# Performance work log

Measured on AMD Instinct MI355X. Metric: run time of the kernel, lower is better.

The kernel has to match this reference:

```python
import jax, jax.numpy as jnp
import numpy as np

B, DIM, H, W = 1, 64, 128, 128
WS = 7  # window_size


def setup_inputs() -> dict:
    key = jax.random.key(0)
    ks = jax.random.split(key, 7)
    scale = 1.0 / np.sqrt(DIM).astype(np.float32)
    x = jax.random.normal(ks[0], (B, DIM, H, W), jnp.float32)
    Wq = jax.random.normal(ks[1], (DIM, DIM), jnp.float32) * scale
    bq = jax.random.normal(ks[2], (DIM,), jnp.float32) * 0.01
    Wk = jax.random.normal(ks[3], (DIM, DIM), jnp.float32) * scale
    bk = jax.random.normal(ks[4], (DIM,), jnp.float32) * 0.01
    Wv = jax.random.normal(ks[5], (DIM, DIM), jnp.float32) * scale
    bv = jax.random.normal(ks[6], (DIM,), jnp.float32) * 0.01
    return {"x": x, "Wq": Wq, "bq": bq, "Wk": Wk, "bk": bk, "Wv": Wv, "bv": bv}


def _conv1x1(x, Wt, b):
    # nn.Conv2d(dim, dim, kernel_size=1): out[b,o,h,w] = sum_c W[o,c]*x[b,c,h,w] + b[o]
    return jnp.einsum('bchw,oc->bohw', x, Wt) + b[None, :, None, None]


def _windows(t, ws):
    # zero-pad then extract ws x ws sliding windows -> (B, C, H, W, ws*ws)
    b, c, h, w = t.shape
    pad = ws // 2
    tp = jnp.pad(t, ((0, 0), (0, 0), (pad, pad), (pad, pad)))
    return jnp.stack([tp[:, :, i:i + h, j:j + w]
                      for i in range(ws) for j in range(ws)], axis=-1)


def reference(x, Wq, bq, Wk, bk, Wv, bv):
    q = _conv1x1(x, Wq, bq)
    k = _conv1x1(x, Wk, bk)
    v = _conv1x1(x, Wv, bv)
    qw = _windows(q, WS)  # (B,C,H,W,P)
    kw = _windows(k, WS)
    vw = _windows(v, WS)
    # row-wise attention: position (h,w) attends to (h,k) over width,
    # contracting channels and window taps p (exact math of the torch einsum)
    attn = jnp.einsum('bchwp,bchkp->bhwk', qw, kw)
    attn = jax.nn.softmax(attn, axis=-1)
    # fuse the weighted sum and the final sum over p into one einsum
    out = jnp.einsum('bhwk,bchkp->bchw', attn, vw)
    return out
```

## Files before the change

### kernel.cpp

```cpp
#include <hip/hip_runtime.h>

static constexpr int C    = 64;
static constexpr int H    = 128;
static constexpr int W    = 128;
static constexpr int NPIX = H * W;
static constexpr int PAD  = 3;

__global__ __launch_bounds__(256, 4) void k_conv(
    const float* __restrict__ x,
    const float* __restrict__ Wq, const float* __restrict__ bq,
    const float* __restrict__ Wk, const float* __restrict__ bk,
    const float* __restrict__ Wv, const float* __restrict__ bv,
    float* __restrict__ qT, float* __restrict__ ko, float* __restrict__ vo)
{
    const int tid  = threadIdx.x;
    const int lane = tid & 63;
    const int p    = blockIdx.x * 64 + lane;
    const int o0   = __builtin_amdgcn_readfirstlane(
                         blockIdx.y * 32 + (tid >> 6) * 8);
    const int z    = blockIdx.z;
    const float* Wm = (z == 0) ? Wq : (z == 1) ? Wk : Wv;
    const float* bm = (z == 0) ? bq : (z == 1) ? bk : bv;

    float xr[C];
#pragma unroll
    for (int c = 0; c < C; ++c) xr[c] = x[c * NPIX + p];

    float acc[8];
#pragma unroll
    for (int j = 0; j < 8; ++j) acc[j] = bm[o0 + j];

#pragma unroll
    for (int c = 0; c < C; ++c) {
        const float xv = xr[c];
#pragma unroll
        for (int j = 0; j < 8; ++j)
            acc[j] += Wm[(o0 + j) * C + c] * xv;
    }

    if (z == 0) {
        *(float4*)(qT + (size_t)p * C + o0) =
            make_float4(acc[0], acc[1], acc[2], acc[3]);
        *(float4*)(qT + (size_t)p * C + o0 + 4) =
            make_float4(acc[4], acc[5], acc[6], acc[7]);
    } else {
        float* outm = (z == 1) ? ko : vo;
#pragma unroll
        for (int j = 0; j < 8; ++j)
            outm[(o0 + j) * NPIX + p] = acc[j];
    }
}

__global__ __launch_bounds__(256, 4) void k_mid(
    const float* __restrict__ qT, const float* __restrict__ kmat,
    const float* __restrict__ v,
    float* __restrict__ Sd, float* __restrict__ Vs)
{
    __shared__ union {
        struct { float Sl[22][130]; float qs[22][64]; } g;
        struct { float vt[22][128]; float vh[22][128]; } box;
    } u;
    const int bid = blockIdx.x;
    const int tid = threadIdx.x;

    if (bid < 1024) {
        const int h   = bid >> 3;
        const int w0  = (bid & 7) * 16;
        const int kk  = tid & 127;
        const int wsl = tid >> 7;

        for (int i = tid; i < 22 * 16; i += 256) {
            int r  = i >> 4, c4 = (i & 15) << 2;
            int wp = w0 - 3 + r;
            float4 qv = make_float4(0.f, 0.f, 0.f, 0.f);
            if (wp >= 0 && wp < W)
                qv = *(const float4*)(qT + (size_t)(h * W + wp) * C + c4);
            *(float4*)(&u.g.qs[r][c4]) = qv;
        }

        float ksr[C];
#pragma unroll
        for (int c = 0; c < C; ++c) ksr[c] = kmat[c * NPIX + h * W + kk];
        __syncthreads();

        for (int j = 0; j < 11; ++j) {
            int row = wsl * 11 + j;
            float a0 = 0.f, a1 = 0.f, a2 = 0.f, a3 = 0.f;
#pragma unroll
            for (int c = 0; c < C; c += 4) {
                float4 qv = *(const float4*)(&u.g.qs[row][c]);
                a0 += qv.x * ksr[c + 0];
                a1 += qv.y * ksr[c + 1];
                a2 += qv.z * ksr[c + 2];
                a3 += qv.w * ksr[c + 3];
            }
            u.g.Sl[row][kk] = (a0 + a1) + (a2 + a3);
        }
        __syncthreads();

#pragma unroll
        for (int r = 0; r < 8; ++r) {
            int wl = wsl * 8 + r;
            float a = 0.f;
#pragma unroll
            for (int dd = -PAD; dd <= PAD; ++dd) {
                int kj = kk + dd;
                if (kj >= 0 && kj < W)
                    a += u.g.Sl[wl + 3 + dd][kj];
            }
            Sd[(size_t)(h * W + w0 + wl) * W + kk] = a;
        }
    } else {
        const int b2 = bid - 1024;
        const int c  = b2 >> 3;
        const int h0 = (b2 & 7) * 16;

        for (int i = tid; i < 22 * 128; i += 256) {
            int r = i >> 7, w = i & 127;
            int h = h0 - 3 + r;
            u.box.vt[r][w] = (h >= 0 && h < H) ? v[c * NPIX + h * W + w] : 0.f;
        }
        __syncthreads();
        for (int i = tid; i < 22 * 128; i += 256) {
            int r = i >> 7, w = i & 127;
            float s = 0.f;
#pragma unroll
            for (int d = -PAD; d <= PAD; ++d) {
                int wj = w + d;
                if (wj >= 0 && wj < W) s += u.box.vt[r][wj];
            }
            u.box.vh[r][w] = s;
        }
        __syncthreads();
        for (int i = tid; i < 16 * 128; i += 256) {
            int r = i >> 7, w = i & 127;
            float s = 0.f;
#pragma unroll
            for (int d = 0; d < 7; ++d) s += u.box.vh[r + d][w];
            Vs[c * NPIX + (h0 + r) * W + w] = s;
        }
    }
}

__global__ __launch_bounds__(256) void k_softmax(
    const float* __restrict__ Sd, float* __restrict__ attn)
{
    __shared__ float Sl[22][132];
    const int w   = blockIdx.x;
    const int h0  = blockIdx.y * 16;
    const int tid = threadIdx.x;

    for (int i = tid; i < 22 * 128; i += 256) {
        int r = i >> 7, kk = i & 127;
        int h = h0 - 3 + r;
        Sl[r][kk] = (h >= 0 && h < H)
                  ? Sd[(size_t)h * NPIX + w * W + kk] : 0.f;
    }
    __syncthreads();

    const int hl  = tid >> 4;
    const int sub = tid & 15;

    float lg[8];
#pragma unroll
    for (int r = 0; r < 8; ++r) {
        int kk = sub + 16 * r;
        float a = 0.f;
#pragma unroll
        for (int d = 0; d < 7; ++d) a += Sl[hl + d][kk];
        lg[r] = a;
    }

    float m = lg[0];
#pragma unroll
    for (int r = 1; r < 8; ++r) m = fmaxf(m, lg[r]);
#pragma unroll
    for (int off = 1; off <= 8; off <<= 1) m = fmaxf(m, __shfl_xor(m, off));
    float ssum = 0.f;
#pragma unroll
    for (int r = 0; r < 8; ++r) { lg[r] = __expf(lg[r] - m); ssum += lg[r]; }
#pragma unroll
    for (int off = 1; off <= 8; off <<= 1) ssum += __shfl_xor(ssum, off);
    float inv = 1.f / ssum;

    float* arow = attn + (size_t)(h0 + hl) * NPIX + (size_t)w * W;
#pragma unroll
    for (int r = 0; r < 8; ++r) arow[sub + 16 * r] = lg[r] * inv;
}

__global__ __launch_bounds__(256) void k_out(
    const float* __restrict__ attn, const float* __restrict__ Vs,
    float* __restrict__ out)
{
    __shared__ float As[W][65];
    const int h   = blockIdx.x;
    const int tid = threadIdx.x;
    const int w   = tid & 127;
    const int c0  = __builtin_amdgcn_readfirstlane(
                        blockIdx.y * 16 + (tid >> 7) * 8);
    const int hb  = h * W;

    float acc[8];
#pragma unroll
    for (int j = 0; j < 8; ++j) acc[j] = 0.f;

    for (int kc = 0; kc < W; kc += 64) {
        __syncthreads();
        for (int i = tid; i < W * 64; i += 256) {
            int kk = i & 63, ww = i >> 6;
            As[ww][kk] = attn[(size_t)h * NPIX + ww * W + kc + kk];
        }
        __syncthreads();
#pragma unroll 4
        for (int kk = 0; kk < 64; ++kk) {
            float a = As[w][kk];
#pragma unroll
            for (int j = 0; j < 8; ++j)
                acc[j] += Vs[(size_t)(c0 + j) * NPIX + hb + kc + kk] * a;
        }
    }

#pragma unroll
    for (int j = 0; j < 8; ++j)
        out[(size_t)(c0 + j) * NPIX + hb + w] = acc[j];
}

extern "C" void kernel_launch(void* const* d_in, const int* in_sizes, int n_in,
                              void* d_out, int out_size, void* d_ws, size_t ws_size,
                              hipStream_t stream)
{
    const float* x  = (const float*)d_in[0];
    const float* Wq = (const float*)d_in[1];
    const float* bq = (const float*)d_in[2];
    const float* Wk = (const float*)d_in[3];
    const float* bk = (const float*)d_in[4];
    const float* Wv = (const float*)d_in[5];
    const float* bv = (const float*)d_in[6];
    float* out = (float*)d_out;

    float* ws = (float*)d_ws;
    const size_t NQ = (size_t)C * NPIX;
    const size_t NS = (size_t)H * W * W;

    float* qT   = ws;
    float* k    = ws + NQ;
    float* v    = ws + 2 * NQ;
    float* Sd   = ws + 3 * NQ;
    float* Vsum = ws + 3 * NQ + NS;
    float* attn = ws + 4 * NQ + NS;

    k_conv<<<dim3(NPIX / 64, 2, 3), 256, 0, stream>>>(x, Wq, bq, Wk, bk, Wv, bv, qT, k, v);
    k_mid<<<dim3(1536), 256, 0, stream>>>(qT, k, v, Sd, Vsum);
    k_softmax<<<dim3(W, H / 16), 256, 0, stream>>>(Sd, attn);
    k_out<<<dim3(H, 4), 256, 0, stream>>>(attn, Vsum, out);
}
```

Measured before the change: 134.3 us.

## Fuse softmax and attention-weighted output into one kernel

Merges the softmax kernel and the output matmul into one kernel. Each block computes the 7-row vertical sum of scores for 64 query positions, applies softmax in registers, writes attention to shared memory, and multiplies by a shared-memory tile of the box-summed V for all 64 channels. This removes the 8 MB attention buffer write and re-read plus one launch. The grid shrinks to 256 blocks of 512 threads, and each block re-reads 7 rows of score data directly from global memory instead of sharing them, which may cost occupancy and some reuse.

Measured after the change: 124.7 us. -7.1%, faster.

```diff
diff --git a/kernel.cpp b/kernel.cpp
--- a/kernel.cpp
+++ b/kernel.cpp
@@ -142,87 +142,93 @@
     }
 }
 
-__global__ __launch_bounds__(256) void k_softmax(
-    const float* __restrict__ Sd, float* __restrict__ attn)
-{
-    __shared__ float Sl[22][132];
-    const int w   = blockIdx.x;
-    const int h0  = blockIdx.y * 16;
+__global__ __launch_bounds__(512, 2) void k_fused(
+    const float* __restrict__ Sd, const float* __restrict__ Vs,
+    float* __restrict__ out)
+{
+    constexpr int AP = 129;
+    __shared__ float At[64][AP];
+    __shared__ float Vl[64][128];
+
+    const int h   = blockIdx.x;
+    const int w0  = blockIdx.y * 64;
     const int tid = threadIdx.x;
 
-    for (int i = tid; i < 22 * 128; i += 256) {
-        int r = i >> 7, kk = i & 127;
-        int h = h0 - 3 + r;
-        Sl[r][kk] = (h >= 0 && h < H)
-                  ? Sd[(size_t)h * NPIX + w * W + kk] : 0.f;
+    float4 vstage[4];
+#pragma unroll
+    for (int r = 0; r < 4; ++r) {
+        int L  = tid + r * 512;
+        int c  = L >> 5;
+        int k4 = (L & 31) << 2;
+        vstage[r] = *(const float4*)(Vs + (size_t)c * NPIX + h * W + k4);
+    }
+
+    const int wl = tid >> 3;
+    const int s  = tid & 7;
+
+    float4 g0 = make_float4(0.f, 0.f, 0.f, 0.f);
+    float4 g1 = g0, g2 = g0, g3 = g0;
+#pragma unroll
+    for (int i = 0; i < 7; ++i) {
+        int hp = h - 3 + i;
+        if (hp >= 0 && hp < H) {
+            const float4* src = (const float4*)(
+                Sd + (size_t)hp * NPIX + (w0 + wl) * W + s * 16);
+            float4 a = src[0], b = src[1], c2 = src[2], d = src[3];
+            g0.x += a.x;  g0.y += a.y;  g0.z += a.z;  g0.w += a.w;
+            g1.x += b.x;  g1.y += b.y;  g1.z += b.z;  g1.w += b.w;
+            g2.x += c2.x; g2.y += c2.y; g2.z += c2.z; g2.w += c2.w;
+            g3.x += d.x;  g3.y += d.y;  g3.z += d.z;  g3.w += d.w;
+        }
+    }
+
+    float lg[16] = { g0.x, g0.y, g0.z, g0.w,  g1.x, g1.y, g1.z, g1.w,
+                     g2.x, g2.y, g2.z, g2.w,  g3.x, g3.y, g3.z, g3.w };
+
+    float m = lg[0];
+#pragma unroll
+    for (int e = 1; e < 16; ++e) m = fmaxf(m, lg[e]);
+#pragma unroll
+    for (int off = 1; off <= 4; off <<= 1) m = fmaxf(m, __shfl_xor(m, off));
+
+    float ssum = 0.f;
+#pragma unroll
+    for (int e = 0; e < 16; ++e) { lg[e] = __expf(lg[e] - m); ssum += lg[e]; }
+#pragma unroll
+    for (int off = 1; off <= 4; off <<= 1) ssum += __shfl_xor(ssum, off);
+    const float inv = 1.f / ssum;
+
+#pragma unroll
+    for (int e = 0; e < 16; ++e) At[wl][s * 16 + e] = lg[e] * inv;
+
+#pragma unroll
+    for (int r = 0; r < 4; ++r) {
+        int L  = tid + r * 512;
+        int c  = L >> 5;
+        int k4 = (L & 31) << 2;
+        *(float4*)(&Vl[c][k4]) = vstage[r];
     }
     __syncthreads();
 
-    const int hl  = tid >> 4;
-    const int sub = tid & 15;
-
-    float lg[8];
-#pragma unroll
-    for (int r = 0; r < 8; ++r) {
-        int kk = sub + 16 * r;
-        float a = 0.f;
-#pragma unroll
-        for (int d = 0; d < 7; ++d) a += Sl[hl + d][kk];
-        lg[r] = a;
-    }
-
-    float m = lg[0];
-#pragma unroll
-    for (int r = 1; r < 8; ++r) m = fmaxf(m, lg[r]);
-#pragma unroll
-    for (int off = 1; off <= 8; off <<= 1) m = fmaxf(m, __shfl_xor(m, off));
-    float ssum = 0.f;
-#pragma unroll
-    for (int r = 0; r < 8; ++r) { lg[r] = __expf(lg[r] - m); ssum += lg[r]; }
-#pragma unroll
-    for (int off = 1; off <= 8; off <<= 1) ssum += __shfl_xor(ssum, off);
-    float inv = 1.f / ssum;
-
-    float* arow = attn + (size_t)(h0 + hl) * NPIX + (size_t)w * W;
-#pragma unroll
-    for (int r = 0; r < 8; ++r) arow[sub + 16 * r] = lg[r] * inv;
-}
-
-__global__ __launch_bounds__(256) void k_out(
-    const float* __restrict__ attn, const float* __restrict__ Vs,
-    float* __restrict__ out)
-{
-    __shared__ float As[W][65];
-    const int h   = blockIdx.x;
-    const int tid = threadIdx.x;
-    const int w   = tid & 127;
-    const int c0  = __builtin_amdgcn_readfirstlane(
-                        blockIdx.y * 16 + (tid >> 7) * 8);
-    const int hb  = h * W;
+    const int w2 = tid & 63;
+    const int c0 = __builtin_amdgcn_readfirstlane((tid >> 6) * 8);
 
     float acc[8];
 #pragma unroll
     for (int j = 0; j < 8; ++j) acc[j] = 0.f;
 
-    for (int kc = 0; kc < W; kc += 64) {
-        __syncthreads();
-        for (int i = tid; i < W * 64; i += 256) {
-            int kk = i & 63, ww = i >> 6;
-            As[ww][kk] = attn[(size_t)h * NPIX + ww * W + kc + kk];
-        }
-        __syncthreads();
-#pragma unroll 4
-        for (int kk = 0; kk < 64; ++kk) {
-            float a = As[w][kk];
-#pragma unroll
-            for (int j = 0; j < 8; ++j)
-                acc[j] += Vs[(size_t)(c0 + j) * NPIX + hb + kc + kk] * a;
+    for (int kk = 0; kk < 128; kk += 4) {
+        float4 a = *(const float4*)(&At[w2][kk]);
+#pragma unroll
+        for (int j = 0; j < 8; ++j) {
+            float4 vv = *(const float4*)(&Vl[c0 + j][kk]);
+            acc[j] += a.x * vv.x + a.y * vv.y + a.z * vv.z + a.w * vv.w;
         }
     }
 
 #pragma unroll
     for (int j = 0; j < 8; ++j)
-        out[(size_t)(c0 + j) * NPIX + hb + w] = acc[j];
+        out[(size_t)(c0 + j) * NPIX + h * W + w0 + w2] = acc[j];
 }
 
 extern "C" void kernel_launch(void* const* d_in, const int* in_sizes, int n_in,
@@ -247,10 +253,8 @@
     float* v    = ws + 2 * NQ;
     float* Sd   = ws + 3 * NQ;
     float* Vsum = ws + 3 * NQ + NS;
-    float* attn = ws + 4 * NQ + NS;
 
     k_conv<<<dim3(NPIX / 64, 2, 3), 256, 0, stream>>>(x, Wq, bq, Wk, bk, Wv, bv, qT, k, v);
     k_mid<<<dim3(1536), 256, 0, stream>>>(qT, k, v, Sd, Vsum);
-    k_softmax<<<dim3(W, H / 16), 256, 0, stream>>>(Sd, attn);
-    k_out<<<dim3(H, 4), 256, 0, stream>>>(attn, Vsum, out);
-}
+    k_fused<<<dim3(H, 2), 512, 0, stream>>>(Sd, Vsum, out);
+}
```
